# Kernel optimization log

Measured on AMD Instinct MI355X. Metric: run time of the kernel, lower is better.

## Reference

```python
import jax, jax.numpy as jnp
import numpy as np

B, S, D, H = 4, 4096, 512, 64

def setup_inputs() -> dict:
    key = jax.random.key(0)
    ks = jax.random.split(key, 7)
    x = jax.random.normal(ks[0], (B, S, D), dtype=jnp.float32)
    Wq = jax.random.normal(ks[1], (D, H), dtype=jnp.float32) / np.sqrt(D)
    bq = jax.random.normal(ks[2], (H,), dtype=jnp.float32) * 0.01
    Wk = jax.random.normal(ks[3], (D, H), dtype=jnp.float32) / np.sqrt(D)
    bk = jax.random.normal(ks[4], (H,), dtype=jnp.float32) * 0.01
    Wv = jax.random.normal(ks[5], (D, H), dtype=jnp.float32) / np.sqrt(D)
    bv = jax.random.normal(ks[6], (H,), dtype=jnp.float32) * 0.01
    return {"x": x, "Wq": Wq, "bq": bq, "Wk": Wk, "bk": bk, "Wv": Wv, "bv": bv}

def reference(x, Wq, bq, Wk, bk, Wv, bv):
    # q,k,v: [B,S,H]
    q = jnp.einsum('bsd,dh->bsh', x, Wq) + bq
    k = jnp.einsum('bsd,dh->bsh', x, Wk) + bk
    v = jnp.einsum('bsd,dh->bsh', x, Wv) + bv
    H_dim = q.shape[-1]
    scores = jnp.einsum('bqh,bkh->bqk', q, k) / jnp.sqrt(jnp.float32(H_dim))  # [B,S,S]
    attn = jax.nn.softmax(scores, axis=-1)
    return jnp.einsum('bqk,bkh->bqh', attn, v)  # [B,S,H]
```

## Files before the change

kernel.cpp:

```cpp
#include <hip/hip_runtime.h>
#include <math.h>

using short8  = __attribute__((ext_vector_type(8))) short;
using floatx4 = __attribute__((ext_vector_type(4))) float;

#define B_DIM 4
#define S_DIM 4096
#define D_DIM 512
#define H_DIM 64
#define NROWS (B_DIM * S_DIM)

#define QSCALE 0.18033688011112042f
#define FMAX   16.0f

__device__ __forceinline__ unsigned short f2bf(float f) {
  unsigned int u = __builtin_bit_cast(unsigned int, f);
  u += 0x7fffu + ((u >> 16) & 1u);
  return (unsigned short)(u >> 16);
}
__device__ __forceinline__ unsigned short f2bf_trunc(float f) {
  return (unsigned short)(__builtin_bit_cast(unsigned int, f) >> 16);
}

#if __has_builtin(__builtin_amdgcn_exp2f)
#define EXP2(x) __builtin_amdgcn_exp2f(x)
#else
#define EXP2(x) exp2f(x)
#endif

__global__ __launch_bounds__(256) void wprep(
    const float* __restrict__ Wq, const float* __restrict__ Wk,
    const float* __restrict__ Wv, unsigned short* __restrict__ Wf)
{
  const int t = blockIdx.x * 256 + threadIdx.x;
  if (t >= 3 * 16 * 4 * 64) return;
  const int lane = t & 63;
  const int f    = t >> 6;
  const int nt   = f & 3;
  const int ks   = (f >> 2) & 15;
  const int pi   = f >> 6;
  const int qq   = lane >> 4;
  const int cc   = lane & 15;
  const float* W = (pi == 0) ? Wq : (pi == 1) ? Wk : Wv;
  const float* src = W + (ks * 32 + qq * 8) * H_DIM + (nt * 16 + cc);
  short8 v;
#pragma unroll
  for (int j = 0; j < 8; ++j) v[j] = (short)f2bf(src[j * H_DIM]);
  *(short8*)(Wf + t * 8) = v;
}

__global__ __launch_bounds__(256, 2) void qkv_proj(
    const float* __restrict__ x, const unsigned short* __restrict__ Wf,
    const float* __restrict__ bq, const float* __restrict__ bk,
    const float* __restrict__ bv,
    unsigned short* __restrict__ Qf, unsigned short* __restrict__ Kf,
    unsigned short* __restrict__ Vf)
{
  __shared__ float PB[2][64][52];
  __shared__ alignas(16) unsigned short QL[32 * 72];
  __shared__ alignas(16) unsigned short KL[32 * 72];
  __shared__ alignas(16) unsigned short VTL[64 * 40];

  const int tid  = threadIdx.x;
  const int lane = tid & 63;
  const int w    = tid >> 6;
  const int qq   = lane >> 4;
  const int cc   = lane & 15;
  const int rh   = w >> 1;
  const int kh   = w & 1;
  const int rowblk = blockIdx.x * 32;

  floatx4 acc[3][4] = {};
  const int arow = rowblk + rh * 16 + cc;
  const float* xrow = x + arow * D_DIM + kh * 256;

#pragma unroll 2
  for (int ks = 0; ks < 8; ++ks) {
    const int ksg = kh * 8 + ks;
    short8 af;
    {
      const float4* xp = (const float4*)(xrow + ks * 32 + qq * 8);
      float4 x0 = xp[0], x1 = xp[1];
      af[0] = (short)f2bf(x0.x); af[1] = (short)f2bf(x0.y);
      af[2] = (short)f2bf(x0.z); af[3] = (short)f2bf(x0.w);
      af[4] = (short)f2bf(x1.x); af[5] = (short)f2bf(x1.y);
      af[6] = (short)f2bf(x1.z); af[7] = (short)f2bf(x1.w);
    }
#pragma unroll
    for (int pi = 0; pi < 3; ++pi) {
#pragma unroll
      for (int nt = 0; nt < 4; ++nt) {
        short8 bfg = *(const short8*)(Wf + (((pi * 16 + ksg) * 4 + nt) * 64 + lane) * 8);
        acc[pi][nt] = __builtin_amdgcn_mfma_f32_16x16x32_bf16(af, bfg, acc[pi][nt], 0, 0, 0);
      }
    }
  }

  if (kh == 1) {
#pragma unroll
    for (int pi = 0; pi < 3; ++pi)
#pragma unroll
      for (int nt = 0; nt < 4; ++nt)
        *(floatx4*)&PB[rh][lane][pi * 16 + nt * 4] = acc[pi][nt];
  }
  __syncthreads();
  if (kh == 0) {
#pragma unroll
    for (int pi = 0; pi < 3; ++pi)
#pragma unroll
      for (int nt = 0; nt < 4; ++nt)
        acc[pi][nt] += *(const floatx4*)&PB[rh][lane][pi * 16 + nt * 4];
#pragma unroll
    for (int nt = 0; nt < 4; ++nt) {
      const int h = nt * 16 + cc;
      const float vbq = bq[h], vbk = bk[h], vbv = bv[h];
#pragma unroll
      for (int r = 0; r < 4; ++r) {
        const int row = rh * 16 + qq * 4 + r;
        QL[row * 72 + h] = f2bf((acc[0][nt][r] + vbq) * QSCALE);
        KL[row * 72 + h] = f2bf(acc[1][nt][r] + vbk);
        VTL[h * 40 + row] = f2bf(acc[2][nt][r] + vbv);
      }
    }
  }
  __syncthreads();

  {
    const int qtl = tid >> 7;
    const int hf  = (tid >> 6) & 1;
    const int lc  = tid & 63;
    const int qqc = lc >> 4, ccc = lc & 15;
    const int gt  = (rowblk >> 4) + qtl;
    short8 vq = *(const short8*)&QL[(qtl * 16 + ccc) * 72 + hf * 32 + qqc * 8];
    *(short8*)(Qf + ((gt * 2 + hf) * 64 + lc) * 8) = vq;
    short8 vk = *(const short8*)&KL[(qtl * 16 + ccc) * 72 + hf * 32 + qqc * 8];
    *(short8*)(Kf + ((gt * 2 + hf) * 64 + lc) * 8) = vk;
  }
  {
    const int nt  = tid >> 6;
    const int qqv = (tid >> 4) & 3;
    const int ccv = tid & 15;
    const int gc  = rowblk >> 6;
    const int hf  = (rowblk >> 5) & 1;
    short8 vv = *(const short8*)&VTL[(nt * 16 + ccv) * 40 + qqv * 8];
    *(short8*)(Vf + (((gc * 8) + nt * 2 + hf) * 64 + qqv * 16 + ccv) * 8) = vv;
  }
}

__global__ __launch_bounds__(512, 2) void flash_attn(
    const unsigned short* __restrict__ Qf, const unsigned short* __restrict__ Kf,
    const unsigned short* __restrict__ Vf, float* __restrict__ out)
{
  __shared__ alignas(16) unsigned short Pl[8][64 * 40];
  __shared__ float OB[4][64 * 65];
  __shared__ float LB[4][64];

  const int tid  = threadIdx.x;
  const int lane = tid & 63;
  const int w    = tid >> 6;
  const int qq   = lane >> 4;
  const int cc   = lane & 15;
  const int b    = blockIdx.x >> 6;
  const int qt64 = blockIdx.x & 63;
  const int qrow0 = qt64 * 64;
  const int gtq  = b * 256 + qt64 * 4;

  short8 aq[4][2];
#pragma unroll
  for (int qs = 0; qs < 4; ++qs)
#pragma unroll
    for (int hf = 0; hf < 2; ++hf)
      aq[qs][hf] = *(const short8*)(Qf + (((gtq + qs) * 2 + hf) * 64 + lane) * 8);

  floatx4 O[4][4] = {};
  float lr[4][4] = {};
  unsigned short* Pw = &Pl[w][0];
  const floatx4 zero = {};
  const int kstart = w * 512;

  short8 bkb[2][2][2], bvb[2][4];
  {
    const int kb = kstart;
    const int kt = b * 256 + (kb >> 4);
    const int vp = (b * 64 + (kb >> 6)) * 8 + ((kb >> 5) & 1);
#pragma unroll
    for (int t = 0; t < 2; ++t)
#pragma unroll
      for (int hf = 0; hf < 2; ++hf)
        bkb[0][t][hf] = *(const short8*)(Kf + (((kt + t) * 2 + hf) * 64 + lane) * 8);
#pragma unroll
    for (int nt = 0; nt < 4; ++nt)
      bvb[0][nt] = *(const short8*)(Vf + ((vp + nt * 2) * 64 + lane) * 8);
  }

#pragma unroll 2
  for (int s = 0; s < 16; ++s) {
    const int cur = s & 1, nxt = cur ^ 1;
    if (s < 15) {
      const int kb = kstart + (s + 1) * 32;
      const int kt = b * 256 + (kb >> 4);
      const int vp = (b * 64 + (kb >> 6)) * 8 + ((kb >> 5) & 1);
#pragma unroll
      for (int t = 0; t < 2; ++t)
#pragma unroll
        for (int hf = 0; hf < 2; ++hf)
          bkb[nxt][t][hf] = *(const short8*)(Kf + (((kt + t) * 2 + hf) * 64 + lane) * 8);
#pragma unroll
      for (int nt = 0; nt < 4; ++nt)
        bvb[nxt][nt] = *(const short8*)(Vf + ((vp + nt * 2) * 64 + lane) * 8);
    }
#pragma unroll
    for (int qs = 0; qs < 4; ++qs) {
      floatx4 s0 = __builtin_amdgcn_mfma_f32_16x16x32_bf16(aq[qs][0], bkb[cur][0][0], zero, 0, 0, 0);
      s0 = __builtin_amdgcn_mfma_f32_16x16x32_bf16(aq[qs][1], bkb[cur][0][1], s0, 0, 0, 0);
      floatx4 s1 = __builtin_amdgcn_mfma_f32_16x16x32_bf16(aq[qs][0], bkb[cur][1][0], zero, 0, 0, 0);
      s1 = __builtin_amdgcn_mfma_f32_16x16x32_bf16(aq[qs][1], bkb[cur][1][1], s1, 0, 0, 0);
#pragma unroll
      for (int r = 0; r < 4; ++r) {
        const int rowoff = (qs * 16 + qq * 4 + r) * 40;
        float p0 = EXP2(s0[r] - FMAX);
        lr[qs][r] += p0;
        Pw[rowoff + cc] = f2bf_trunc(p0);
        float p1 = EXP2(s1[r] - FMAX);
        lr[qs][r] += p1;
        Pw[rowoff + 16 + cc] = f2bf_trunc(p1);
      }
    }
#pragma unroll
    for (int qs = 0; qs < 4; ++qs) {
      const short8 ap = *(const short8*)&Pw[(qs * 16 + cc) * 40 + qq * 8];
#pragma unroll
      for (int nt = 0; nt < 4; ++nt)
        O[qs][nt] = __builtin_amdgcn_mfma_f32_16x16x32_bf16(ap, bvb[cur][nt], O[qs][nt], 0, 0, 0);
    }
  }

#pragma unroll
  for (int qs = 0; qs < 4; ++qs)
#pragma unroll
    for (int r = 0; r < 4; ++r) {
      float v = lr[qs][r];
      v += __shfl_xor(v, 1); v += __shfl_xor(v, 2);
      v += __shfl_xor(v, 4); v += __shfl_xor(v, 8);
      lr[qs][r] = v;
    }

  if (w >= 4) {
    float* Ob = OB[w - 4];
#pragma unroll
    for (int qs = 0; qs < 4; ++qs)
#pragma unroll
      for (int nt = 0; nt < 4; ++nt)
#pragma unroll
        for (int r = 0; r < 4; ++r)
          Ob[(qs * 16 + qq * 4 + r) * 65 + nt * 16 + cc] = O[qs][nt][r];
    if (cc == 0)
#pragma unroll
      for (int qs = 0; qs < 4; ++qs)
#pragma unroll
        for (int r = 0; r < 4; ++r) LB[w - 4][qs * 16 + qq * 4 + r] = lr[qs][r];
  }
  __syncthreads();
  if (w < 4) {
    const float* Ob = OB[w];
#pragma unroll
    for (int qs = 0; qs < 4; ++qs)
#pragma unroll
      for (int nt = 0; nt < 4; ++nt)
#pragma unroll
        for (int r = 0; r < 4; ++r)
          O[qs][nt][r] += Ob[(qs * 16 + qq * 4 + r) * 65 + nt * 16 + cc];
#pragma unroll
    for (int qs = 0; qs < 4; ++qs)
#pragma unroll
      for (int r = 0; r < 4; ++r) lr[qs][r] += LB[w][qs * 16 + qq * 4 + r];
  }
  __syncthreads();
  if (w == 2 || w == 3) {
    float* Ob = OB[w - 2];
#pragma unroll
    for (int qs = 0; qs < 4; ++qs)
#pragma unroll
      for (int nt = 0; nt < 4; ++nt)
#pragma unroll
        for (int r = 0; r < 4; ++r)
          Ob[(qs * 16 + qq * 4 + r) * 65 + nt * 16 + cc] = O[qs][nt][r];
    if (cc == 0)
#pragma unroll
      for (int qs = 0; qs < 4; ++qs)
#pragma unroll
        for (int r = 0; r < 4; ++r) LB[w - 2][qs * 16 + qq * 4 + r] = lr[qs][r];
  }
  __syncthreads();
  if (w < 2) {
    const float* Ob = OB[w];
#pragma unroll
    for (int qs = 0; qs < 4; ++qs)
#pragma unroll
      for (int nt = 0; nt < 4; ++nt)
#pragma unroll
        for (int r = 0; r < 4; ++r)
          O[qs][nt][r] += Ob[(qs * 16 + qq * 4 + r) * 65 + nt * 16 + cc];
#pragma unroll
    for (int qs = 0; qs < 4; ++qs)
#pragma unroll
      for (int r = 0; r < 4; ++r) lr[qs][r] += LB[w][qs * 16 + qq * 4 + r];
  }
  __syncthreads();
  if (w == 1) {
    float* Ob = OB[0];
#pragma unroll
    for (int qs = 0; qs < 4; ++qs)
#pragma unroll
      for (int nt = 0; nt < 4; ++nt)
#pragma unroll
        for (int r = 0; r < 4; ++r)
          Ob[(qs * 16 + qq * 4 + r) * 65 + nt * 16 + cc] = O[qs][nt][r];
    if (cc == 0)
#pragma unroll
      for (int qs = 0; qs < 4; ++qs)
#pragma unroll
        for (int r = 0; r < 4; ++r) LB[0][qs * 16 + qq * 4 + r] = lr[qs][r];
  }
  __syncthreads();
  if (w == 0) {
    const float* Ob = OB[0];
#pragma unroll
    for (int qs = 0; qs < 4; ++qs) {
#pragma unroll
      for (int r = 0; r < 4; ++r) {
        const float lt  = lr[qs][r] + LB[0][qs * 16 + qq * 4 + r];
        const float inv = 1.0f / lt;
        const int rowg  = b * S_DIM + qrow0 + qs * 16 + qq * 4 + r;
#pragma unroll
        for (int nt = 0; nt < 4; ++nt) {
          const float o = O[qs][nt][r] + Ob[(qs * 16 + qq * 4 + r) * 65 + nt * 16 + cc];
          out[rowg * H_DIM + nt * 16 + cc] = o * inv;
        }
      }
    }
  }
}

extern "C" void kernel_launch(void* const* d_in, const int* in_sizes, int n_in,
                              void* d_out, int out_size, void* d_ws, size_t ws_size,
                              hipStream_t stream) {
  const float* x  = (const float*)d_in[0];
  const float* Wq = (const float*)d_in[1];
  const float* bq = (const float*)d_in[2];
  const float* Wk = (const float*)d_in[3];
  const float* bk = (const float*)d_in[4];
  const float* Wv = (const float*)d_in[5];
  const float* bv = (const float*)d_in[6];
  float* out = (float*)d_out;

  unsigned short* Qf = (unsigned short*)d_ws;
  unsigned short* Kf = Qf + NROWS * H_DIM;
  unsigned short* Vf = Kf + NROWS * H_DIM;
  unsigned short* Wf = Vf + NROWS * H_DIM;

  wprep<<<48, 256, 0, stream>>>(Wq, Wk, Wv, Wf);
  qkv_proj<<<512, 256, 0, stream>>>(x, Wf, bq, bk, bv, Qf, Kf, Vf);
  flash_attn<<<256, 512, 0, stream>>>(Qf, Kf, Vf, out);
}
```

Before: 135.0 us.

## Pack P pairs, compute row sums via MFMA, prefetch projection operands, remap blocks

Several changes at once. The projection kernel double-buffers the W fragment and x loads one k-step ahead. The attention kernel packs two bf16 probabilities into one 32-bit LDS store with a byte permute, and the V layout is permuted to match the new P column order. Row sums now come from an extra MFMA against a ones vector, replacing per-element adds and the shuffle reduction. Block indices are also remapped across batches. The trade is more registers for the prefetch buffers and one extra MFMA per query subtile, and the row sums now accumulate the bf16-rounded probabilities.

```diff
diff --git a/kernel.cpp b/kernel.cpp
--- a/kernel.cpp
+++ b/kernel.cpp
@@ -18,8 +18,15 @@
   u += 0x7fffu + ((u >> 16) & 1u);
   return (unsigned short)(u >> 16);
 }
-__device__ __forceinline__ unsigned short f2bf_trunc(float f) {
-  return (unsigned short)(__builtin_bit_cast(unsigned int, f) >> 16);
+
+__device__ __forceinline__ unsigned int pack_bf2(float lo, float hi) {
+#if __has_builtin(__builtin_amdgcn_perm)
+  return __builtin_amdgcn_perm(__builtin_bit_cast(unsigned int, hi),
+                               __builtin_bit_cast(unsigned int, lo), 0x07060302u);
+#else
+  return (__builtin_bit_cast(unsigned int, hi) & 0xFFFF0000u) |
+         (__builtin_bit_cast(unsigned int, lo) >> 16);
+#endif
 }
 
 #if __has_builtin(__builtin_amdgcn_exp2f)
@@ -74,26 +81,46 @@
   const int arow = rowblk + rh * 16 + cc;
   const float* xrow = x + arow * D_DIM + kh * 256;
 
-#pragma unroll 2
+  short8 wb[2][12];
+  float4 xb[2][2];
+
+  {
+    const int ksg = kh * 8;
+#pragma unroll
+    for (int pi = 0; pi < 3; ++pi)
+#pragma unroll
+      for (int nt = 0; nt < 4; ++nt)
+        wb[0][pi * 4 + nt] = *(const short8*)(Wf + (((pi * 16 + ksg) * 4 + nt) * 64 + lane) * 8);
+    const float4* xp = (const float4*)(xrow + qq * 8);
+    xb[0][0] = xp[0]; xb[0][1] = xp[1];
+  }
+
+#pragma unroll
   for (int ks = 0; ks < 8; ++ks) {
-    const int ksg = kh * 8 + ks;
+    const int cur = ks & 1;
+    if (ks < 7) {
+      const int ksg = kh * 8 + ks + 1;
+#pragma unroll
+      for (int pi = 0; pi < 3; ++pi)
+#pragma unroll
+        for (int nt = 0; nt < 4; ++nt)
+          wb[cur ^ 1][pi * 4 + nt] = *(const short8*)(Wf + (((pi * 16 + ksg) * 4 + nt) * 64 + lane) * 8);
+      const float4* xp = (const float4*)(xrow + (ks + 1) * 32 + qq * 8);
+      xb[cur ^ 1][0] = xp[0]; xb[cur ^ 1][1] = xp[1];
+    }
     short8 af;
     {
-      const float4* xp = (const float4*)(xrow + ks * 32 + qq * 8);
-      float4 x0 = xp[0], x1 = xp[1];
+      float4 x0 = xb[cur][0], x1 = xb[cur][1];
       af[0] = (short)f2bf(x0.x); af[1] = (short)f2bf(x0.y);
       af[2] = (short)f2bf(x0.z); af[3] = (short)f2bf(x0.w);
       af[4] = (short)f2bf(x1.x); af[5] = (short)f2bf(x1.y);
       af[6] = (short)f2bf(x1.z); af[7] = (short)f2bf(x1.w);
     }
 #pragma unroll
-    for (int pi = 0; pi < 3; ++pi) {
-#pragma unroll
-      for (int nt = 0; nt < 4; ++nt) {
-        short8 bfg = *(const short8*)(Wf + (((pi * 16 + ksg) * 4 + nt) * 64 + lane) * 8);
-        acc[pi][nt] = __builtin_amdgcn_mfma_f32_16x16x32_bf16(af, bfg, acc[pi][nt], 0, 0, 0);
-      }
-    }
+    for (int pi = 0; pi < 3; ++pi)
+#pragma unroll
+      for (int nt = 0; nt < 4; ++nt)
+        acc[pi][nt] = __builtin_amdgcn_mfma_f32_16x16x32_bf16(af, wb[cur][pi * 4 + nt], acc[pi][nt], 0, 0, 0);
   }
 
   if (kh == 1) {
@@ -142,7 +169,10 @@
     const int ccv = tid & 15;
     const int gc  = rowblk >> 6;
     const int hf  = (rowblk >> 5) & 1;
-    short8 vv = *(const short8*)&VTL[(nt * 16 + ccv) * 40 + qqv * 8];
+    short8 vv;
+#pragma unroll
+    for (int j = 0; j < 8; ++j)
+      vv[j] = (short)VTL[(nt * 16 + ccv) * 40 + qqv * 4 + (j >> 1) + ((j & 1) << 4)];
     *(short8*)(Vf + (((gc * 8) + nt * 2 + hf) * 64 + qqv * 16 + ccv) * 8) = vv;
   }
 }
@@ -151,7 +181,7 @@
     const unsigned short* __restrict__ Qf, const unsigned short* __restrict__ Kf,
     const unsigned short* __restrict__ Vf, float* __restrict__ out)
 {
-  __shared__ alignas(16) unsigned short Pl[8][64 * 40];
+  __shared__ alignas(16) unsigned int Pl[8][64 * 20];
   __shared__ float OB[4][64 * 65];
   __shared__ float LB[4][64];
 
@@ -160,8 +190,9 @@
   const int w    = tid >> 6;
   const int qq   = lane >> 4;
   const int cc   = lane & 15;
-  const int b    = blockIdx.x >> 6;
-  const int qt64 = blockIdx.x & 63;
+  const int g    = blockIdx.x;
+  const int b    = (g & 7) >> 1;
+  const int qt64 = ((g >> 3) << 1) | (g & 1);
   const int qrow0 = qt64 * 64;
   const int gtq  = b * 256 + qt64 * 4;
 
@@ -172,9 +203,14 @@
     for (int hf = 0; hf < 2; ++hf)
       aq[qs][hf] = *(const short8*)(Qf + (((gtq + qs) * 2 + hf) * 64 + lane) * 8);
 
+  short8 vone;
+#pragma unroll
+  for (int j = 0; j < 8; ++j) vone[j] = (short)0x3F80;
+
   floatx4 O[4][4] = {};
-  float lr[4][4] = {};
-  unsigned short* Pw = &Pl[w][0];
+  floatx4 O5[4] = {};
+  unsigned int* Pw = &Pl[w][0];
+  const unsigned short* Pr = (const unsigned short*)Pw;
   const floatx4 zero = {};
   const int kstart = w * 512;
 
@@ -217,33 +253,26 @@
       s1 = __builtin_amdgcn_mfma_f32_16x16x32_bf16(aq[qs][1], bkb[cur][1][1], s1, 0, 0, 0);
 #pragma unroll
       for (int r = 0; r < 4; ++r) {
-        const int rowoff = (qs * 16 + qq * 4 + r) * 40;
         float p0 = EXP2(s0[r] - FMAX);
-        lr[qs][r] += p0;
-        Pw[rowoff + cc] = f2bf_trunc(p0);
         float p1 = EXP2(s1[r] - FMAX);
-        lr[qs][r] += p1;
-        Pw[rowoff + 16 + cc] = f2bf_trunc(p1);
+        Pw[(qs * 16 + qq * 4 + r) * 20 + cc] = pack_bf2(p0, p1);
       }
     }
 #pragma unroll
     for (int qs = 0; qs < 4; ++qs) {
-      const short8 ap = *(const short8*)&Pw[(qs * 16 + cc) * 40 + qq * 8];
+      const short8 ap = *(const short8*)(Pr + (qs * 16 + cc) * 40 + qq * 8);
 #pragma unroll
       for (int nt = 0; nt < 4; ++nt)
         O[qs][nt] = __builtin_amdgcn_mfma_f32_16x16x32_bf16(ap, bvb[cur][nt], O[qs][nt], 0, 0, 0);
-    }
-  }
-
+      O5[qs] = __builtin_amdgcn_mfma_f32_16x16x32_bf16(ap, vone, O5[qs], 0, 0, 0);
+    }
+  }
+
+  float lr[4][4];
 #pragma unroll
   for (int qs = 0; qs < 4; ++qs)
 #pragma unroll
-    for (int r = 0; r < 4; ++r) {
-      float v = lr[qs][r];
-      v += __shfl_xor(v, 1); v += __shfl_xor(v, 2);
-      v += __shfl_xor(v, 4); v += __shfl_xor(v, 8);
-      lr[qs][r] = v;
-    }
+    for (int r = 0; r < 4; ++r) lr[qs][r] = O5[qs][r];
 
   if (w >= 4) {
     float* Ob = OB[w - 4];
```

After: 116.8 us. 1.16x faster.
